# Kernel tuning notes

Hardware: AMD Instinct MI355X
Metric: run time of the kernel (lower is better)

Reference implementation:

```python
import jax, jax.numpy as jnp
import numpy as np

NUM_HEADS = 8
NUM_GROUPS = 32
EPS = 1e-5
RESCALE = 1.0


def setup_inputs() -> dict:
    key = jax.random.key(0)
    ks = jax.random.split(key, 7)
    b, c, h, w = 16, 512, 32, 32
    return {
        "x": jax.random.normal(ks[0], (b, c, h, w), jnp.float32),
        "norm_w": jax.random.normal(ks[1], (c,), jnp.float32),
        "norm_b": jax.random.normal(ks[2], (c,), jnp.float32),
        "qkv_w": jax.random.normal(ks[3], (3 * c, c), jnp.float32) * (c ** -0.5),
        "qkv_b": jax.random.normal(ks[4], (3 * c,), jnp.float32) * 0.02,
        "proj_w": jax.random.normal(ks[5], (c, c), jnp.float32) * (c ** -0.5),
        "proj_b": jax.random.normal(ks[6], (c,), jnp.float32) * 0.02,
    }


def _group_norm(x, w, b):
    # x: [B, C, L]
    B, C, L = x.shape
    g = x.reshape(B, NUM_GROUPS, (C // NUM_GROUPS) * L)
    mu = jnp.mean(g, axis=-1, keepdims=True)
    var = jnp.var(g, axis=-1, keepdims=True)
    g = (g - mu) * jax.lax.rsqrt(var + EPS)
    return g.reshape(B, C, L) * w[None, :, None] + b[None, :, None]


def reference(x, norm_w, norm_b, qkv_w, qkv_b, proj_w, proj_b):
    b, c, hh, ww = x.shape
    L = hh * ww
    H = NUM_HEADS
    ch = c // H  # head dim

    xr = x.reshape(b, c, L)
    hid = _group_norm(xr, norm_w, norm_b)

    # 1x1 conv1d == matmul over channel dim: [3c, c] @ [b, c, L]
    qkv = jnp.einsum('oc,bcl->bol', qkv_w, hid) + qkv_b[None, :, None]
    # torch: reshape(b*H, 3*ch, L).split(ch) -> per-head contiguous [q|k|v] blocks
    qkv = qkv.reshape(b, H, 3, ch, L)
    q, k, v = qkv[:, :, 0], qkv[:, :, 1], qkv[:, :, 2]  # [b, H, ch, L]

    scale = 1.0 / (ch ** 0.25)
    weight = jnp.einsum('bhct,bhcs->bhts', q * scale, k * scale)
    weight = jax.nn.softmax(weight.astype(jnp.float32), axis=-1).astype(weight.dtype)
    a = jnp.einsum('bhts,bhcs->bhct', weight, v)  # [b, H, ch, L]

    h = a.reshape(b, c, L)
    h = jnp.einsum('oc,bcl->bol', proj_w, h) + proj_b[None, :, None]
    h = h.reshape(b, c, hh, ww)
    return (x + h) / RESCALE
```

## Files before the change

kernel.cpp:

```cpp
#include <hip/hip_runtime.h>
#include <hip/hip_bf16.h>
#include <stdint.h>


using f32x4  = __attribute__((ext_vector_type(4))) float;
using bf16x8 = __attribute__((ext_vector_type(8))) __bf16;
using s8v    = __attribute__((ext_vector_type(8))) short;
using s4v    = __attribute__((ext_vector_type(4))) short;

__device__ __forceinline__ short f2bf(float f){
  union { float f; unsigned u; } c; c.f = f;
  unsigned r = (c.u + 0x7FFFu + ((c.u >> 16) & 1u)) >> 16;
  return (short)r;
}

__device__ __forceinline__ float exp2_fast(float x){
#if __has_builtin(__builtin_amdgcn_exp2f)
  return __builtin_amdgcn_exp2f(x);
#else
  return exp2f(x);
#endif
}

__device__ __forceinline__ void gl_lds16(const void* g, void* l){
  __builtin_amdgcn_global_load_lds((const __attribute__((address_space(1))) void*)g,
                                   (__attribute__((address_space(3))) void*)l, 16, 0, 0);
}

__global__ void k_convw(const float* __restrict__ qw, const float* __restrict__ pw,
                        short* __restrict__ qwb, short* __restrict__ pwb){
  int i = blockIdx.x * 256 + threadIdx.x;
  if (i < 1536*512) qwb[i] = f2bf(qw[i]);
  else              pwb[i - 1536*512] = f2bf(pw[i - 1536*512]);
}

__global__ __launch_bounds__(256) void k_gnorm(const float* __restrict__ x,
                                               const float* __restrict__ w,
                                               const float* __restrict__ bia,
                                               short* __restrict__ hid){
  int b = blockIdx.x >> 5;
  int g = blockIdx.x & 31;
  int tid = threadIdx.x;
  const float* xg = x + ((size_t)b*512 + g*16)*1024;
  int l0 = tid * 4;
  float v[16][4];
  float s1 = 0.f, s2 = 0.f;
  #pragma unroll
  for (int c = 0; c < 16; c++){
    f32x4 t = *(const f32x4*)(xg + c*1024 + l0);
    #pragma unroll
    for (int j = 0; j < 4; j++){ v[c][j] = t[j]; s1 += t[j]; s2 += t[j]*t[j]; }
  }
  #pragma unroll
  for (int m = 32; m; m >>= 1){ s1 += __shfl_xor(s1, m); s2 += __shfl_xor(s2, m); }
  __shared__ float r1[4], r2[4];
  int wv = tid >> 6, ln = tid & 63;
  if (ln == 0){ r1[wv] = s1; r2[wv] = s2; }
  __syncthreads();
  s1 = r1[0]+r1[1]+r1[2]+r1[3];
  s2 = r2[0]+r2[1]+r2[2]+r2[3];
  float mu = s1 * (1.f/16384.f);
  float var = s2 * (1.f/16384.f) - mu*mu;
  float rs = rsqrtf(var + 1e-5f);
  float ww[16], bb[16];
  #pragma unroll
  for (int c = 0; c < 16; c++){ ww[c] = w[g*16+c]*rs; bb[c] = bia[g*16+c]; }
  #pragma unroll
  for (int j = 0; j < 4; j++){
    short o[16];
    #pragma unroll
    for (int c = 0; c < 16; c++) o[c] = f2bf((v[c][j]-mu)*ww[c] + bb[c]);
    short* dst = hid + ((size_t)(b*1024 + l0 + j))*512 + g*16;
    *(s8v*)dst     = *(s8v*)o;
    *(s8v*)(dst+8) = *(s8v*)(o+8);
  }
}

template<int EPI>
__global__ __launch_bounds__(256) void k_gemm(
    const short* __restrict__ A, const short* __restrict__ Bm,
    const float* __restrict__ bias, const float* __restrict__ xres,
    short* __restrict__ q_t, short* __restrict__ k_t, short* __restrict__ v_t,
    float* __restrict__ outp)
{
  __shared__ short Al[2][128*64];
  __shared__ short Bl[2][128*64];
  int id = blockIdx.x;
  int xcd = id & 7, ix = id >> 3;
  int n0 = (xcd + 8*(ix & 15)) * 128;
  int m0 = (ix >> 4) * 128;
  int tid = threadIdx.x;
  int lane = tid & 63;
  int wv = tid >> 6;
  int wr = wv >> 1, wc = wv & 1;
  f32x4 acc[4][4] = {};

  auto STAGE = [&](int db, int k0){
    #pragma unroll
    for (int i = 0; i < 8; i++){
      int cc = wv*8 + i;
      if (cc < 16){
        int slot = cc*64 + lane;
        int row = slot >> 3, off = slot & 7;
        gl_lds16(A + (size_t)(m0+row)*512 + k0 + (off ^ (row&7))*8,
                 (char*)Al[db] + cc*1024);
      } else {
        int slot = (cc-16)*64 + lane;
        int row = slot >> 3, off = slot & 7;
        gl_lds16(Bm + (size_t)(n0+row)*512 + k0 + (off ^ (row&7))*8,
                 (char*)Bl[db] + (cc-16)*1024);
      }
    }
  };

  STAGE(0, 0);
  for (int t = 0; t < 8; t++){
    STAGE((t+1)&1, ((t+1)&7)*64);
    asm volatile("s_waitcnt vmcnt(8)" ::: "memory");
    __builtin_amdgcn_s_barrier();
    int db = t & 1;
    #pragma unroll
    for (int kk = 0; kk < 2; kk++){
      bf16x8 af[4], bf[4];
      #pragma unroll
      for (int m = 0; m < 4; m++){
        int row = wr*64 + m*16 + (lane&15);
        int byte = row*128 + (((kk*64) + ((lane>>4)*16)) ^ ((row&7)<<4));
        af[m] = *(const bf16x8*)((char*)Al[db] + byte);
      }
      #pragma unroll
      for (int n = 0; n < 4; n++){
        int row = wc*64 + n*16 + (lane&15);
        int byte = row*128 + (((kk*64) + ((lane>>4)*16)) ^ ((row&7)<<4));
        bf[n] = *(const bf16x8*)((char*)Bl[db] + byte);
      }
      __builtin_amdgcn_s_setprio(1);
      #pragma unroll
      for (int m = 0; m < 4; m++)
        #pragma unroll
        for (int n = 0; n < 4; n++)
          acc[m][n] = __builtin_amdgcn_mfma_f32_16x16x32_bf16(af[m], bf[n], acc[m][n], 0, 0, 0);
      __builtin_amdgcn_s_setprio(0);
    }
    __builtin_amdgcn_s_barrier();
  }

  if (EPI == 0){
    #pragma unroll
    for (int m = 0; m < 4; m++){
      int ob  = m0 + wr*64 + m*16 + ((lane>>4)<<2);
      int hh  = ob / 192;
      int rem = ob % 192;
      int sel = rem >> 6;
      int c0  = rem & 63;
      float bs[4];
      #pragma unroll
      for (int r = 0; r < 4; r++) bs[r] = bias[ob+r];
      #pragma unroll
      for (int n = 0; n < 4; n++){
        int nn = n0 + wc*64 + n*16 + (lane&15);
        int bb = nn >> 10, ll = nn & 1023;
        int bh = bb*8 + hh;
        if (sel == 2){
          int sl = ll & 63;
          short* p0 = v_t + ((size_t)bh*16 + (ll>>6))*4096
                    + (((sl>>4)*4 + ((sl>>2)&3))*4 + (c0>>4))*64 + (c0&15)*4 + (sl&3);
          #pragma unroll
          for (int r = 0; r < 4; r++) p0[r*4] = f2bf(acc[m][n][r] + bs[r]);
        } else {
          float sc = (sel == 0) ? 0.18033688011112042f : 1.0f;
          short o4[4];
          #pragma unroll
          for (int r = 0; r < 4; r++) o4[r] = f2bf((acc[m][n][r] + bs[r]) * sc);
          short* dst = (sel == 0 ? q_t : k_t) + ((size_t)bh*1024 + ll)*64 + c0;
          *(s4v*)dst = *(s4v*)o4;
        }
      }
    }
  } else {
    #pragma unroll
    for (int m = 0; m < 4; m++){
      int ob = m0 + wr*64 + m*16 + ((lane>>4)<<2);
      float bs[4];
      #pragma unroll
      for (int r = 0; r < 4; r++) bs[r] = bias[ob+r];
      #pragma unroll
      for (int n = 0; n < 4; n++){
        int nn = n0 + wc*64 + n*16 + (lane&15);
        int bb = nn >> 10, ll = nn & 1023;
        #pragma unroll
        for (int r = 0; r < 4; r++){
          size_t idx = ((size_t)bb*512 + ob + r)*1024 + ll;
          outp[idx] = xres[idx] + acc[m][n][r] + bs[r];
        }
      }
    }
  }
}

__global__ __launch_bounds__(256, 4) void k_attn(
    const short* __restrict__ q_t, const short* __restrict__ k_t,
    const short* __restrict__ v_t, short* __restrict__ a_bt)
{
  __shared__ short Kl[2][64*64];
  __shared__ short Vl[2][64*64];
  int id = blockIdx.x;
  int xcd = id & 7, ix = id >> 3;
  int bh = xcd*16 + (ix >> 3);
  int qb = ix & 7;
  int bb = bh >> 3, hh = bh & 7;
  int tid = threadIdx.x;
  int lane = tid & 63;
  int wv = tid >> 6;
  int l15 = lane & 15, g = lane >> 4;

  bf16x8 qf[2][2];
  #pragma unroll
  for (int qt = 0; qt < 2; qt++){
    const short* qbase = q_t + ((size_t)bh*1024 + qb*128 + qt*64 + wv*16 + l15)*64 + g*8;
    qf[qt][0] = *(const bf16x8*)(qbase);
    qf[qt][1] = *(const bf16x8*)(qbase + 32);
  }
  asm volatile("" :: "v"(qf[0][0]), "v"(qf[0][1]), "v"(qf[1][0]), "v"(qf[1][1]));

  bf16x8 onesb;
  #pragma unroll
  for (int i = 0; i < 8; i++) onesb[i] = (__bf16)1.0f;

  auto STAGE = [&](int db, int s0){
    #pragma unroll
    for (int i = 0; i < 4; i++){
      int cc = wv*4 + i;
      if (cc < 8){
        int slot = cc*64 + lane;
        int row = slot >> 3, off = slot & 7;
        gl_lds16(k_t + ((size_t)bh*1024 + s0 + row)*64 + (off ^ (row&7))*8,
                 (char*)Kl[db] + cc*1024);
      } else {
        gl_lds16(v_t + ((size_t)bh*16 + (s0>>6))*4096 + (cc-8)*512 + lane*8,
                 (char*)Vl[db] + (cc-8)*1024);
      }
    }
  };

  f32x4 o[2][4] = {};
  f32x4 osum[2] = {};

  STAGE(0, 0);
  for (int t = 0; t < 16; t++){
    STAGE((t+1)&1, ((t+1)&15)*64);
    asm volatile("s_waitcnt vmcnt(4)" ::: "memory");
    __builtin_amdgcn_s_barrier();
    int db = t & 1;

    f32x4 sc[2][4] = {};
    #pragma unroll
    for (int j = 0; j < 4; j++){
      #pragma unroll
      for (int ks = 0; ks < 2; ks++){
        int row = j*16 + l15;
        int byte = row*128 + (((ks*64) + (g*16)) ^ ((row&7)<<4));
        bf16x8 kf = *(const bf16x8*)((char*)Kl[db] + byte);
        __builtin_amdgcn_s_setprio(1);
        #pragma unroll
        for (int qt = 0; qt < 2; qt++)
          sc[qt][j] = __builtin_amdgcn_mfma_f32_16x16x32_bf16(kf, qf[qt][ks], sc[qt][j], 0, 0, 0);
        __builtin_amdgcn_s_setprio(0);
      }
    }

    #pragma unroll
    for (int ks = 0; ks < 2; ks++){
      bf16x8 pa[2];
      #pragma unroll
      for (int qt = 0; qt < 2; qt++){
        #pragma unroll
        for (int i2 = 0; i2 < 8; i2++)
          pa[qt][i2] = (__bf16)exp2_fast(sc[qt][2*ks + (i2>>2)][i2&3]);
        osum[qt] = __builtin_amdgcn_mfma_f32_16x16x32_bf16(pa[qt], onesb, osum[qt], 0, 0, 0);
      }
      #pragma unroll
      for (int jd = 0; jd < 4; jd++){
        union { s4v h[2]; bf16x8 b; } vb;
        vb.h[0] = *(const s4v*)((char*)Vl[db] + ks*4096        + g*512 + jd*128 + l15*8);
        vb.h[1] = *(const s4v*)((char*)Vl[db] + ks*4096 + 2048 + g*512 + jd*128 + l15*8);
        __builtin_amdgcn_s_setprio(1);
        #pragma unroll
        for (int qt = 0; qt < 2; qt++)
          o[qt][jd] = __builtin_amdgcn_mfma_f32_16x16x32_bf16(pa[qt], vb.b, o[qt][jd], 0, 0, 0);
        __builtin_amdgcn_s_setprio(0);
      }
    }
    __builtin_amdgcn_s_barrier();
  }

  #pragma unroll
  for (int qt = 0; qt < 2; qt++){
    #pragma unroll
    for (int r = 0; r < 4; r++){
      float inv = 1.f / osum[qt][r];
      int qrow = qb*128 + qt*64 + wv*16 + g*4 + r;
      #pragma unroll
      for (int jd = 0; jd < 4; jd++)
        a_bt[((size_t)bb*1024 + qrow)*512 + hh*64 + jd*16 + l15] = f2bf(o[qt][jd][r] * inv);
    }
  }
}

extern "C" void kernel_launch(void* const* d_in, const int* in_sizes, int n_in,
                              void* d_out, int out_size, void* d_ws, size_t ws_size,
                              hipStream_t stream){
  const float* x  = (const float*)d_in[0];
  const float* nw = (const float*)d_in[1];
  const float* nb = (const float*)d_in[2];
  const float* qw = (const float*)d_in[3];
  const float* qb = (const float*)d_in[4];
  const float* pw = (const float*)d_in[5];
  const float* pb = (const float*)d_in[6];
  float* outp = (float*)d_out;

  char* ws = (char*)d_ws;
  short* hid  = (short*)(ws);
  short* qwb  = (short*)(ws + 16777216);
  short* pwb  = (short*)(ws + 18350080);
  short* q_t  = (short*)(ws + 18874368);
  short* k_t  = (short*)(ws + 35651584);
  short* v_t  = (short*)(ws + 52428800);
  short* a_bt = hid;
  if (ws_size < 69206016) return;

  k_convw<<<4096, 256, 0, stream>>>(qw, pw, qwb, pwb);
  k_gnorm<<<512, 256, 0, stream>>>(x, nw, nb, hid);
  k_gemm<0><<<1536, 256, 0, stream>>>(qwb, hid, qb, nullptr, q_t, k_t, v_t, nullptr);
  k_attn<<<1024, 256, 0, stream>>>(q_t, k_t, v_t, a_bt);
  k_gemm<1><<<512, 256, 0, stream>>>(pwb, a_bt, pb, x, nullptr, nullptr, nullptr, outp);
}
```

Baseline: 131.1 us.

## Permute QKV weight rows by q/k/v and stage V epilogue through LDS

The QKV weight and bias rows are reordered during bf16 conversion so that each 128-row M tile holds only q, only k, or only v. The GEMM epilogue can then take a single branch per block. V tiles are transposed through shared memory and written out as coalesced 16-byte stores, replacing the earlier scattered 2-byte stores. The block-index mapping now walks M-tiles fastest, and the last k-step skips the redundant prefetch. The permuted bias is stored temporarily in the output buffer, which the final GEMM later overwrites.

```diff
diff --git a/kernel.cpp b/kernel.cpp
--- a/kernel.cpp
+++ b/kernel.cpp
@@ -28,10 +28,23 @@
 }
 
 __global__ void k_convw(const float* __restrict__ qw, const float* __restrict__ pw,
-                        short* __restrict__ qwb, short* __restrict__ pwb){
+                        const float* __restrict__ qb,
+                        short* __restrict__ qwb, short* __restrict__ pwb,
+                        float* __restrict__ qbp){
   int i = blockIdx.x * 256 + threadIdx.x;
-  if (i < 1536*512) qwb[i] = f2bf(qw[i]);
-  else              pwb[i - 1536*512] = f2bf(pw[i - 1536*512]);
+  if (i < 786432){
+    int o = i >> 9, kk = i & 511;
+    int h = o / 192, rem = o - h*192;
+    int nr = (rem >> 6)*512 + h*64 + (rem & 63);
+    qwb[nr*512 + kk] = f2bf(qw[i]);
+  } else if (i < 1048576){
+    int j = i - 786432;
+    pwb[j] = f2bf(pw[j]);
+  } else if (i < 1050112){
+    int o = i - 1048576;
+    int h = o / 192, rem = o - h*192;
+    qbp[(rem >> 6)*512 + h*64 + (rem & 63)] = qb[o];
+  }
 }
 
 __global__ __launch_bounds__(256) void k_gnorm(const float* __restrict__ x,
@@ -87,12 +100,16 @@
   __shared__ short Bl[2][128*64];
   int id = blockIdx.x;
   int xcd = id & 7, ix = id >> 3;
-  int n0 = (xcd + 8*(ix & 15)) * 128;
-  int m0 = (ix >> 4) * 128;
+  int mt, nt;
+  if (EPI == 0){ mt = ix % 12; nt = ix / 12; }
+  else         { mt = ix & 3;  nt = ix >> 2; }
+  int m0 = mt * 128;
+  int n0 = (xcd + 8*nt) * 128;
   int tid = threadIdx.x;
   int lane = tid & 63;
   int wv = tid >> 6;
   int wr = wv >> 1, wc = wv & 1;
+  int l15 = lane & 15, g = lane >> 4;
   f32x4 acc[4][4] = {};
 
   auto STAGE = [&](int db, int k0){
@@ -115,8 +132,12 @@
 
   STAGE(0, 0);
   for (int t = 0; t < 8; t++){
-    STAGE((t+1)&1, ((t+1)&7)*64);
-    asm volatile("s_waitcnt vmcnt(8)" ::: "memory");
+    if (t < 7){
+      STAGE((t+1)&1, (t+1)*64);
+      asm volatile("s_waitcnt vmcnt(8)" ::: "memory");
+    } else {
+      asm volatile("s_waitcnt vmcnt(0)" ::: "memory");
+    }
     __builtin_amdgcn_s_barrier();
     int db = t & 1;
     #pragma unroll
@@ -124,14 +145,14 @@
       bf16x8 af[4], bf[4];
       #pragma unroll
       for (int m = 0; m < 4; m++){
-        int row = wr*64 + m*16 + (lane&15);
-        int byte = row*128 + (((kk*64) + ((lane>>4)*16)) ^ ((row&7)<<4));
+        int row = wr*64 + m*16 + l15;
+        int byte = row*128 + (((kk*64) + (g*16)) ^ ((row&7)<<4));
         af[m] = *(const bf16x8*)((char*)Al[db] + byte);
       }
       #pragma unroll
       for (int n = 0; n < 4; n++){
-        int row = wc*64 + n*16 + (lane&15);
-        int byte = row*128 + (((kk*64) + ((lane>>4)*16)) ^ ((row&7)<<4));
+        int row = wc*64 + n*16 + l15;
+        int byte = row*128 + (((kk*64) + (g*16)) ^ ((row&7)<<4));
         bf[n] = *(const bf16x8*)((char*)Bl[db] + byte);
       }
       __builtin_amdgcn_s_setprio(1);
@@ -146,47 +167,69 @@
   }
 
   if (EPI == 0){
-    #pragma unroll
-    for (int m = 0; m < 4; m++){
-      int ob  = m0 + wr*64 + m*16 + ((lane>>4)<<2);
-      int hh  = ob / 192;
-      int rem = ob % 192;
-      int sel = rem >> 6;
-      int c0  = rem & 63;
-      float bs[4];
-      #pragma unroll
-      for (int r = 0; r < 4; r++) bs[r] = bias[ob+r];
-      #pragma unroll
-      for (int n = 0; n < 4; n++){
-        int nn = n0 + wc*64 + n*16 + (lane&15);
-        int bb = nn >> 10, ll = nn & 1023;
-        int bh = bb*8 + hh;
-        if (sel == 2){
-          int sl = ll & 63;
-          short* p0 = v_t + ((size_t)bh*16 + (ll>>6))*4096
-                    + (((sl>>4)*4 + ((sl>>2)&3))*4 + (c0>>4))*64 + (c0&15)*4 + (sl&3);
-          #pragma unroll
-          for (int r = 0; r < 4; r++) p0[r*4] = f2bf(acc[m][n][r] + bs[r]);
-        } else {
-          float sc = (sel == 0) ? 0.18033688011112042f : 1.0f;
+    int sel = m0 >> 9;
+    if (sel < 2){
+      const float sc = (sel == 0) ? 0.18033688011112042f : 1.0f;
+      short* dstb = (sel == 0) ? q_t : k_t;
+      #pragma unroll
+      for (int m = 0; m < 4; m++){
+        int ob = m0 + wr*64 + m*16 + (g<<2);
+        int hh = (ob>>6)&7, c0 = ob&63;
+        float bs[4];
+        #pragma unroll
+        for (int r = 0; r < 4; r++) bs[r] = bias[ob+r];
+        #pragma unroll
+        for (int n = 0; n < 4; n++){
+          int nn = n0 + wc*64 + n*16 + l15;
+          int bb = nn >> 10, ll = nn & 1023;
+          int bh = bb*8 + hh;
           short o4[4];
           #pragma unroll
           for (int r = 0; r < 4; r++) o4[r] = f2bf((acc[m][n][r] + bs[r]) * sc);
-          short* dst = (sel == 0 ? q_t : k_t) + ((size_t)bh*1024 + ll)*64 + c0;
-          *(s4v*)dst = *(s4v*)o4;
+          *(s4v*)(dstb + ((size_t)bh*1024 + ll)*64 + c0) = *(s4v*)o4;
         }
       }
+    } else {
+      short* Sc = (short*)Al;
+      #pragma unroll
+      for (int m = 0; m < 4; m++){
+        int ob = m0 + wr*64 + m*16 + (g<<2);
+        int h2 = (ob>>6)&1, cq = (ob>>4)&3;
+        float bs[4];
+        #pragma unroll
+        for (int r = 0; r < 4; r++) bs[r] = bias[ob+r];
+        #pragma unroll
+        for (int n = 0; n < 4; n++){
+          int nn = n0 + wc*64 + n*16 + l15;
+          int sl = nn & 63, sreg = (nn>>6)&1;
+          int base = (h2*2 + sreg)*4096 + ((sl>>2)*4 + cq)*64 + (sl&3);
+          #pragma unroll
+          for (int r = 0; r < 4; r++)
+            Sc[base + (4*g + r)*4] = f2bf(acc[m][n][r] + bs[r]);
+        }
+      }
+      __syncthreads();
+      int b0  = n0 >> 10;
+      int s64 = (n0 >> 6) & 15;
+      int hb  = (m0 - 1024) >> 6;
+      #pragma unroll
+      for (int it = 0; it < 8; it++){
+        int flat = it*2048 + tid*8;
+        int h2 = flat >> 13, rem = flat & 8191, sreg = rem >> 12, off = rem & 4095;
+        int bh = b0*8 + hb + h2;
+        *(s8v*)(v_t + ((size_t)bh*16 + s64 + sreg)*4096 + off) = *(const s8v*)(Sc + flat);
+      }
     }
   } else {
     #pragma unroll
     for (int m = 0; m < 4; m++){
-      int ob = m0 + wr*64 + m*16 + ((lane>>4)<<2);
+      int ob = m0 + wr*64 + m*16 + (g<<2);
       float bs[4];
       #pragma unroll
       for (int r = 0; r < 4; r++) bs[r] = bias[ob+r];
       #pragma unroll
       for (int n = 0; n < 4; n++){
-        int nn = n0 + wc*64 + n*16 + (lane&15);
+        int nn = n0 + wc*64 + n*16 + l15;
         int bb = nn >> 10, ll = nn & 1023;
         #pragma unroll
         for (int r = 0; r < 4; r++){
@@ -327,11 +370,12 @@
   short* k_t  = (short*)(ws + 35651584);
   short* v_t  = (short*)(ws + 52428800);
   short* a_bt = hid;
+  float* qbp  = (float*)d_out;
   if (ws_size < 69206016) return;
 
-  k_convw<<<4096, 256, 0, stream>>>(qw, pw, qwb, pwb);
+  k_convw<<<4103, 256, 0, stream>>>(qw, pw, qb, qwb, pwb, qbp);
   k_gnorm<<<512, 256, 0, stream>>>(x, nw, nb, hid);
-  k_gemm<0><<<1536, 256, 0, stream>>>(qwb, hid, qb, nullptr, q_t, k_t, v_t, nullptr);
+  k_gemm<0><<<1536, 256, 0, stream>>>(qwb, hid, qbp, nullptr, q_t, k_t, v_t, nullptr);
   k_attn<<<1024, 256, 0, stream>>>(q_t, k_t, v_t, a_bt);
   k_gemm<1><<<512, 256, 0, stream>>>(pwb, a_bt, pb, x, nullptr, nullptr, nullptr, outp);
 }
```

Result: faster. 126.9 us (-3.2%).
